# Performance work log

Measured on AMD Instinct MI355X. Metric: run time of the kernel, lower is better.

Reference implementation:

```python
import jax, jax.numpy as jnp
import numpy as np

N = 100000
E = 1200000
F_IN, HID, LAT = 16, 128, 64
G = 8  # number of graphs
SG_K = 4


def setup_inputs() -> dict:
    key = jax.random.key(0)
    ks = jax.random.split(key, 20)
    x = jax.random.normal(ks[0], (N, F_IN), dtype=jnp.float32)
    edge_index = jax.random.randint(ks[1], (2, E), 0, N, dtype=jnp.int64)
    batch = jnp.sort(jax.random.randint(ks[2], (N,), 0, G, dtype=jnp.int64))

    def lin(k, fan_in, fan_out):
        s = 1.0 / np.sqrt(fan_in)
        k1, k2 = jax.random.split(k)
        W = jax.random.uniform(k1, (fan_in, fan_out), jnp.float32, -s, s)
        b = jax.random.uniform(k2, (fan_out,), jnp.float32, -s, s)
        return W, b

    W1, b1 = lin(ks[3], F_IN, HID)
    W2, b2 = lin(ks[4], HID, LAT)
    Wg1, bg1 = lin(ks[5], LAT, LAT)
    Wg2, bg2 = lin(ks[6], LAT, LAT)
    Wg3, bg3 = lin(ks[7], LAT, LAT)
    Wsg, bsg = lin(ks[8], LAT, LAT)
    Wf1, bf1 = lin(ks[9], LAT, 32)
    Wf2, bf2 = lin(ks[10], 32, 16)
    Wc, bc = lin(ks[11], 16, 1)
    Wcb, bcb = lin(ks[12], 16, 1)
    return dict(x=x, edge_index=edge_index, batch=batch,
                W1=W1, b1=b1, W2=W2, b2=b2,
                Wg1=Wg1, bg1=bg1, Wg2=Wg2, bg2=bg2, Wg3=Wg3, bg3=bg3,
                Wsg=Wsg, bsg=bsg, Wf1=Wf1, bf1=bf1, Wf2=Wf2, bf2=bf2,
                Wc=Wc, bc=bc, Wcb=Wcb, bcb=bcb)


def reference(x, edge_index, batch,
              W1, b1, W2, b2,
              Wg1, bg1, Wg2, bg2, Wg3, bg3,
              Wsg, bsg, Wf1, bf1, Wf2, bf2,
              Wc, bc, Wcb, bcb):
    n = x.shape[0]
    loops = jnp.arange(n, dtype=edge_index.dtype)
    src = jnp.concatenate([edge_index[0], loops])  # add self-loops (PyG default)
    dst = jnp.concatenate([edge_index[1], loops])
    deg = jax.ops.segment_sum(jnp.ones_like(dst, jnp.float32), dst, num_segments=n)
    dis = jnp.where(deg > 0, jax.lax.rsqrt(jnp.maximum(deg, 1.0)), 0.0)
    norm = dis[src] * dis[dst]  # symmetric GCN normalization

    def prop(h):
        # D^{-1/2} (A+I) D^{-1/2} h  via gather -> scale -> scatter-add
        return jax.ops.segment_sum(h[src] * norm[:, None], dst, num_segments=n)

    def gcn(h, W, b):
        return prop(h @ W) + b

    # encoder
    z = jax.nn.relu(gcn(x, W1, b1))
    z = gcn(z, W2, b2)
    # stacked GCNs
    z = jax.nn.relu(gcn(z, Wg1, bg1))
    z = jax.nn.relu(gcn(z, Wg2, bg2))
    z = jax.nn.relu(gcn(z, Wg3, bg3))
    # SGConv: propagate K times, then linear
    h = z
    for _ in range(SG_K):
        h = prop(h)
    z = h @ Wsg + bsg
    # global max pool per graph
    g = jax.ops.segment_max(z, batch, num_segments=G)
    g = jax.nn.relu(g @ Wf1 + bf1)
    g = jax.nn.relu(g @ Wf2 + bf2)
    cpd_pred = g @ Wc + bc
    comb_logits = g @ Wcb + bcb
    return cpd_pred, comb_logits
```

## Files before the change

kernel.cpp:

```cpp
#include <hip/hip_runtime.h>
#include <hip/hip_bf16.h>
#include <hip/hip_fp16.h>
#include <math.h>

#define G_GRAPHS 8

__device__ __forceinline__ unsigned fmap(float f) {
    unsigned b = __float_as_uint(f);
    return (b & 0x80000000u) ? ~b : (b | 0x80000000u);
}
__device__ __forceinline__ float funmap(unsigned u) {
    unsigned b = (u & 0x80000000u) ? (u & 0x7fffffffu) : ~u;
    return __uint_as_float(b);
}
__device__ __forceinline__ void fma_row(float wv, uint2 r,
                                        float& ax, float& ay, float& az, float& aw) {
    float2 f01 = __half22float2(*(__half2*)&r.x);
    float2 f23 = __half22float2(*(__half2*)&r.y);
    ax += wv * f01.x; ay += wv * f01.y; az += wv * f23.x; aw += wv * f23.y;
}
__device__ __forceinline__ uint2 pack4(float ax, float ay, float az, float aw) {
    __half2 p01 = __float22half2_rn(make_float2(ax, ay));
    __half2 p23 = __float22half2_rn(make_float2(az, aw));
    uint2 r;
    r.x = *(unsigned*)&p01;
    r.y = *(unsigned*)&p23;
    return r;
}

__global__ void k_count(const int* __restrict__ dst, int* __restrict__ deg, int E) {
    int e = blockIdx.x * 256 + threadIdx.x;
    if (e < E) atomicAdd(&deg[dst[e]], 1);
}

__global__ void k_dis(const int* __restrict__ deg, float* __restrict__ dis, int N) {
    int i = blockIdx.x * 256 + threadIdx.x;
    if (i < N) dis[i] = rsqrtf((float)(deg[i] + 1));
}

__global__ void k_scanA(const int* __restrict__ deg, int* __restrict__ rowst,
                        int* __restrict__ bsum, int N) {
    __shared__ int s[256];
    int i = blockIdx.x * 256 + threadIdx.x;
    int v = (i < N) ? deg[i] : 0;
    s[threadIdx.x] = v;
    __syncthreads();
    for (int off = 1; off < 256; off <<= 1) {
        int t = (threadIdx.x >= off) ? s[threadIdx.x - off] : 0;
        __syncthreads();
        s[threadIdx.x] += t;
        __syncthreads();
    }
    if (i < N) rowst[i] = s[threadIdx.x] - v;
    if (threadIdx.x == 255) bsum[blockIdx.x] = s[255];
}

__global__ void k_scanB(int* __restrict__ bsum, int NB) {
    __shared__ int s[512];
    int t = threadIdx.x;
    int v = (t < NB) ? bsum[t] : 0;
    s[t] = v;
    __syncthreads();
    for (int off = 1; off < 512; off <<= 1) {
        int x = (t >= off) ? s[t - off] : 0;
        __syncthreads();
        s[t] += x;
        __syncthreads();
    }
    if (t < NB) bsum[t] = s[t] - v;
}

__global__ void k_scanC(int* __restrict__ rowst, const int* __restrict__ bsum, int N) {
    int i = blockIdx.x * 256 + threadIdx.x;
    if (i < N) rowst[i] += bsum[blockIdx.x];
}

__global__ void k_fill(const int* __restrict__ src, const int* __restrict__ dst,
                       const float* __restrict__ dis, const int* __restrict__ rowst,
                       int* __restrict__ cnt, int2* __restrict__ edge, int E) {
    int e = blockIdx.x * 256 + threadIdx.x;
    if (e >= E) return;
    int d = dst[e], s = src[e];
    int p = rowst[d] + atomicAdd(&cnt[d], 1);
    edge[p] = make_int2(s, __float_as_int(dis[s] * dis[d]));
}

__global__ void k_x2h(const float* __restrict__ x, __half* __restrict__ xh, int n4) {
    int i = blockIdx.x * 256 + threadIdx.x;
    if (i >= n4) return;
    float4 v = ((const float4*)x)[i];
    ((uint2*)xh)[i] = pack4(v.x, v.y, v.z, v.w);
}

__global__ __launch_bounds__(256) void k_prop16(
        const __half* __restrict__ xh, float* __restrict__ out,
        const float* __restrict__ dis, const int* __restrict__ rowst,
        const int* __restrict__ deg, const int2* __restrict__ edge, int N) {
    int t = threadIdx.x, lane = t & 63, w = t >> 6;
    int grp = lane >> 2, sub = lane & 3;
    int node = blockIdx.x * 64 + w * 16 + grp;
    if (node >= N) return;
    const uint2* xr = (const uint2*)xh;
    float d = dis[node];
    float sc = d * d;
    float ax = 0.f, ay = 0.f, az = 0.f, aw = 0.f;
    fma_row(sc, xr[node * 4 + sub], ax, ay, az, aw);
    int s = rowst[node], dg = deg[node];
    const int2* ep = edge + s;
    int i = 0;
    for (; i + 3 < dg; i += 4) {
        int2 e0 = ep[i], e1 = ep[i + 1], e2 = ep[i + 2], e3 = ep[i + 3];
        uint2 r0 = xr[e0.x * 4 + sub];
        uint2 r1 = xr[e1.x * 4 + sub];
        uint2 r2 = xr[e2.x * 4 + sub];
        uint2 r3 = xr[e3.x * 4 + sub];
        fma_row(__int_as_float(e0.y), r0, ax, ay, az, aw);
        fma_row(__int_as_float(e1.y), r1, ax, ay, az, aw);
        fma_row(__int_as_float(e2.y), r2, ax, ay, az, aw);
        fma_row(__int_as_float(e3.y), r3, ax, ay, az, aw);
    }
    for (; i < dg; ++i) {
        int2 e0 = ep[i];
        fma_row(__int_as_float(e0.y), xr[e0.x * 4 + sub], ax, ay, az, aw);
    }
    ((float4*)out)[node * 4 + sub] = make_float4(ax, ay, az, aw);
}

__global__ __launch_bounds__(256) void k_dense(
        const float* __restrict__ p0, __half* __restrict__ out,
        const float* __restrict__ W1, const float* __restrict__ b1,
        const float* __restrict__ W2, int N) {
    __shared__ float zT[4][128][4];
    int t = threadIdx.x, lane = t & 63, w = t >> 6;
    int base = (blockIdx.x * 4 + w) * 4;
    if (base >= N) return;
    float p = p0[base * 16 + lane];
    float zA[4], zB[4];
    float bA = b1[lane], bB = b1[lane + 64];
    #pragma unroll
    for (int j = 0; j < 4; ++j) { zA[j] = bA; zB[j] = bB; }
    #pragma unroll
    for (int k = 0; k < 16; ++k) {
        float w1a = W1[k * 128 + lane];
        float w1b = W1[k * 128 + lane + 64];
        #pragma unroll
        for (int j = 0; j < 4; ++j) {
            float pk = __shfl(p, j * 16 + k);
            zA[j] += pk * w1a;
            zB[j] += pk * w1b;
        }
    }
    #pragma unroll
    for (int j = 0; j < 4; ++j) {
        zT[w][lane][j]      = fmaxf(zA[j], 0.f);
        zT[w][lane + 64][j] = fmaxf(zB[j], 0.f);
    }
    float acc[4] = {0.f, 0.f, 0.f, 0.f};
    #pragma unroll 4
    for (int k = 0; k < 128; ++k) {
        float wk = W2[k * 64 + lane];
        float4 zk = *(const float4*)&zT[w][k][0];
        acc[0] += zk.x * wk; acc[1] += zk.y * wk;
        acc[2] += zk.z * wk; acc[3] += zk.w * wk;
    }
    #pragma unroll
    for (int j = 0; j < 4; ++j)
        if (base + j < N) out[(base + j) * 64 + lane] = __float2half(acc[j]);
}

__global__ __launch_bounds__(256) void k_prop64(
        const __half* __restrict__ in, __half* __restrict__ out,
        const float* __restrict__ dis, const int* __restrict__ rowst,
        const int* __restrict__ deg, const int2* __restrict__ edge,
        const float* __restrict__ bias, int relu,
        const float* __restrict__ W, const float* __restrict__ gbias, int N) {
    __shared__ float Wlds[64 * 64];
    __shared__ float zbuf[4][2][64];
    int t = threadIdx.x, lane = t & 63, w = t >> 6;
    int q = lane & 15, g = lane >> 4;
    const uint2* inr = (const uint2*)in;
    if (W) {
        for (int i = t; i < 64 * 64 / 4; i += 256)
            ((float4*)Wlds)[i] = ((const float4*)W)[i];
        __syncthreads();
    }
    float4 b4 = make_float4(0.f, 0.f, 0.f, 0.f);
    if (bias) b4 = ((const float4*)bias)[q];
    float gb = (W && gbias) ? gbias[lane] : 0.f;
    int wid = blockIdx.x * 4 + w;
    const int stride = gridDim.x * 4 * 2;
    for (int n0 = wid * 2; n0 < N; n0 += stride) {
        int n1 = n0 + 1;
        bool h1 = n1 < N;
        int s0 = rowst[n0], d0 = deg[n0];
        int s1 = h1 ? rowst[n1] : s0, d1 = h1 ? deg[n1] : 0;
        float di0 = dis[n0];
        float di1 = h1 ? dis[n1] : 0.f;
        const int2* e0 = edge + s0;
        const int2* e1 = edge + s1;
        float sc0 = di0 * di0 * 0.25f, sc1 = di1 * di1 * 0.25f;
        float a0x = 0.f, a0y = 0.f, a0z = 0.f, a0w = 0.f;
        float a1x = 0.f, a1y = 0.f, a1z = 0.f, a1w = 0.f;
        fma_row(sc0, inr[n0 * 16 + q], a0x, a0y, a0z, a0w);
        fma_row(sc1, inr[(h1 ? n1 : n0) * 16 + q], a1x, a1y, a1z, a1w);
        int m = d0 > d1 ? d0 : d1;
        for (int base = 0; base < m; base += 16) {
            int i0 = base + g, i1 = i0 + 4, i2 = i0 + 8, i3 = i0 + 12;
            int2 ma0 = e0[(i0 < d0) ? i0 : 0];
            int2 ma1 = e0[(i1 < d0) ? i1 : 0];
            int2 ma2 = e0[(i2 < d0) ? i2 : 0];
            int2 ma3 = e0[(i3 < d0) ? i3 : 0];
            int2 mb0 = e1[(i0 < d1) ? i0 : 0];
            int2 mb1 = e1[(i1 < d1) ? i1 : 0];
            int2 mb2 = e1[(i2 < d1) ? i2 : 0];
            int2 mb3 = e1[(i3 < d1) ? i3 : 0];
            uint2 ra0 = inr[ma0.x * 16 + q];
            uint2 ra1 = inr[ma1.x * 16 + q];
            uint2 ra2 = inr[ma2.x * 16 + q];
            uint2 ra3 = inr[ma3.x * 16 + q];
            uint2 rb0 = inr[mb0.x * 16 + q];
            uint2 rb1 = inr[mb1.x * 16 + q];
            uint2 rb2 = inr[mb2.x * 16 + q];
            uint2 rb3 = inr[mb3.x * 16 + q];
            float wa0 = (i0 < d0) ? __int_as_float(ma0.y) : 0.f;
            float wa1 = (i1 < d0) ? __int_as_float(ma1.y) : 0.f;
            float wa2 = (i2 < d0) ? __int_as_float(ma2.y) : 0.f;
            float wa3 = (i3 < d0) ? __int_as_float(ma3.y) : 0.f;
            float wb0 = (i0 < d1) ? __int_as_float(mb0.y) : 0.f;
            float wb1 = (i1 < d1) ? __int_as_float(mb1.y) : 0.f;
            float wb2 = (i2 < d1) ? __int_as_float(mb2.y) : 0.f;
            float wb3 = (i3 < d1) ? __int_as_float(mb3.y) : 0.f;
            fma_row(wa0, ra0, a0x, a0y, a0z, a0w);
            fma_row(wa1, ra1, a0x, a0y, a0z, a0w);
            fma_row(wa2, ra2, a0x, a0y, a0z, a0w);
            fma_row(wa3, ra3, a0x, a0y, a0z, a0w);
            fma_row(wb0, rb0, a1x, a1y, a1z, a1w);
            fma_row(wb1, rb1, a1x, a1y, a1z, a1w);
            fma_row(wb2, rb2, a1x, a1y, a1z, a1w);
            fma_row(wb3, rb3, a1x, a1y, a1z, a1w);
        }
        a0x += __shfl_xor(a0x,16); a0y += __shfl_xor(a0y,16); a0z += __shfl_xor(a0z,16); a0w += __shfl_xor(a0w,16);
        a0x += __shfl_xor(a0x,32); a0y += __shfl_xor(a0y,32); a0z += __shfl_xor(a0z,32); a0w += __shfl_xor(a0w,32);
        a1x += __shfl_xor(a1x,16); a1y += __shfl_xor(a1y,16); a1z += __shfl_xor(a1z,16); a1w += __shfl_xor(a1w,16);
        a1x += __shfl_xor(a1x,32); a1y += __shfl_xor(a1y,32); a1z += __shfl_xor(a1z,32); a1w += __shfl_xor(a1w,32);
        a0x += b4.x; a0y += b4.y; a0z += b4.z; a0w += b4.w;
        a1x += b4.x; a1y += b4.y; a1z += b4.z; a1w += b4.w;
        if (relu) {
            a0x = fmaxf(a0x,0.f); a0y = fmaxf(a0y,0.f); a0z = fmaxf(a0z,0.f); a0w = fmaxf(a0w,0.f);
            a1x = fmaxf(a1x,0.f); a1y = fmaxf(a1y,0.f); a1z = fmaxf(a1z,0.f); a1w = fmaxf(a1w,0.f);
        }
        if (!W) {
            if (g == 0) {
                ((uint2*)out)[n0 * 16 + q] = pack4(a0x, a0y, a0z, a0w);
                if (h1) ((uint2*)out)[n1 * 16 + q] = pack4(a1x, a1y, a1z, a1w);
            }
        } else {
            if (g == 0) {
                ((float4*)zbuf[w][0])[q] = make_float4(a0x, a0y, a0z, a0w);
                ((float4*)zbuf[w][1])[q] = make_float4(a1x, a1y, a1z, a1w);
            }
            float acc0 = gb, acc1 = gb;
            for (int k = 0; k < 64; ++k) {
                float wk = Wlds[k * 64 + lane];
                acc0 += zbuf[w][0][k] * wk;
                acc1 += zbuf[w][1][k] * wk;
            }
            out[n0 * 64 + lane] = __float2half(acc0);
            if (h1) out[n1 * 64 + lane] = __float2half(acc1);
        }
    }
}

__global__ void k_pool_init(unsigned* __restrict__ gmax) {
    gmax[blockIdx.x * 64 + threadIdx.x] = fmap(-INFINITY);
}

__global__ void k_pool(const __half* __restrict__ z, const int* __restrict__ batch,
                       unsigned* __restrict__ gmax, int N) {
    int f = threadIdx.x & 63, w = threadIdx.x >> 6;
    int base = (blockIdx.x * 4 + w) * 32;
    if (base >= N) return;
    int end = base + 32; if (end > N) end = N;
    int b0 = batch[base], b1 = batch[end - 1];
    if (b0 == b1) {
        float lmax = -INFINITY;
        for (int n = base; n < end; ++n)
            lmax = fmaxf(lmax, __half2float(z[n * 64 + f]));
        atomicMax(&gmax[b0 * 64 + f], fmap(lmax));
    } else {
        int curb = b0; float lmax = -INFINITY;
        for (int n = base; n < end; ++n) {
            int b = batch[n];
            if (b != curb) {
                atomicMax(&gmax[curb * 64 + f], fmap(lmax));
                curb = b; lmax = -INFINITY;
            }
            lmax = fmaxf(lmax, __half2float(z[n * 64 + f]));
        }
        atomicMax(&gmax[curb * 64 + f], fmap(lmax));
    }
}

__global__ void k_head(const unsigned* __restrict__ gmax,
                       const float* __restrict__ Wf1, const float* __restrict__ bf1,
                       const float* __restrict__ Wf2, const float* __restrict__ bf2,
                       const float* __restrict__ Wc, const float* __restrict__ bc,
                       const float* __restrict__ Wcb, const float* __restrict__ bcb,
                       float* __restrict__ out) {
    __shared__ float g[8][64], h1[8][32], h2[8][16];
    int t = threadIdx.x;
    for (int i = t; i < 512; i += 64) g[i >> 6][i & 63] = funmap(gmax[i]);
    __syncthreads();
    for (int i = t; i < 256; i += 64) {
        int r = i >> 5, c = i & 31;
        float a = bf1[c];
        for (int k = 0; k < 64; ++k) a += g[r][k] * Wf1[k * 32 + c];
        h1[r][c] = fmaxf(a, 0.f);
    }
    __syncthreads();
    for (int i = t; i < 128; i += 64) {
        int r = i >> 4, c = i & 15;
        float a = bf2[c];
        for (int k = 0; k < 32; ++k) a += h1[r][k] * Wf2[k * 16 + c];
        h2[r][c] = fmaxf(a, 0.f);
    }
    __syncthreads();
    if (t < 16) {
        int r = t & 7;
        bool comb = t >= 8;
        const float* W = comb ? Wcb : Wc;
// ... 12 lines not shown
    const float* W1   = (const float*)d_in[3];
    const float* b1   = (const float*)d_in[4];
    const float* W2   = (const float*)d_in[5];
    const float* b2   = (const float*)d_in[6];
    const float* Wg1  = (const float*)d_in[7];
    const float* bg1  = (const float*)d_in[8];
    const float* Wg2  = (const float*)d_in[9];
    const float* bg2  = (const float*)d_in[10];
    const float* Wg3  = (const float*)d_in[11];
    const float* bg3  = (const float*)d_in[12];
    const float* Wsg  = (const float*)d_in[13];
    const float* bsg  = (const float*)d_in[14];
    const float* Wf1  = (const float*)d_in[15];
    const float* bf1  = (const float*)d_in[16];
    const float* Wf2  = (const float*)d_in[17];
    const float* bf2  = (const float*)d_in[18];
    const float* Wc   = (const float*)d_in[19];
    const float* bc   = (const float*)d_in[20];
    const float* Wcb  = (const float*)d_in[21];
    const float* bcb  = (const float*)d_in[22];

    const int N = in_sizes[0] / 16;
    const int E = in_sizes[1] / 2;
    const int* esrc = ei;
    const int* edst = ei + E;

    char* ws = (char*)d_ws;
    auto alloc = [&](size_t bytes) -> char* {
        char* p = ws;
        ws += (bytes + 255) & ~(size_t)255;
        return p;
    };
    int*      deg   = (int*)alloc((size_t)N * 4);
    int*      cnt   = (int*)alloc((size_t)N * 4);
    int*      rowst = (int*)alloc((size_t)(N + 1) * 4);
    int*      bsum  = (int*)alloc(4096);
    float*    dis   = (float*)alloc((size_t)N * 4);
    int2*     edge  = (int2*)alloc((size_t)(E + 16) * 8);
    __half*   xh    = (__half*)alloc((size_t)N * 16 * 2);
    float*    p0    = (float*)alloc((size_t)N * 16 * 4);
    __half*   bufA  = (__half*)alloc((size_t)N * 64 * 2);
    __half*   bufB  = (__half*)alloc((size_t)N * 64 * 2);
    unsigned* gmax  = (unsigned*)alloc((size_t)G_GRAPHS * 64 * 4);

    hipMemsetAsync(deg, 0, (size_t)N * 4, stream);
    hipMemsetAsync(cnt, 0, (size_t)N * 4, stream);
    hipMemsetAsync(edge + E, 0, 16 * 8, stream);

    const int EB = (E + 255) / 256;
    const int NB = (N + 255) / 256;
    const int PB = 2048;

    k_count<<<EB, 256, 0, stream>>>(edst, deg, E);
    k_dis<<<NB, 256, 0, stream>>>(deg, dis, N);
    k_scanA<<<NB, 256, 0, stream>>>(deg, rowst, bsum, N);
    k_scanB<<<1, 512, 0, stream>>>(bsum, NB);
    k_scanC<<<NB, 256, 0, stream>>>(rowst, bsum, N);
    k_fill<<<EB, 256, 0, stream>>>(esrc, edst, dis, rowst, cnt, edge, E);
    k_x2h<<<(N * 4 + 255) / 256, 256, 0, stream>>>(x, xh, N * 4);

    k_prop16<<<(N + 63) / 64, 256, 0, stream>>>(xh, p0, dis, rowst, deg, edge, N);
    k_dense<<<(N + 15) / 16, 256, 0, stream>>>(p0, bufA, W1, b1, W2, N);
    k_prop64<<<PB, 256, 0, stream>>>(bufA, bufB, dis, rowst, deg, edge, b2, 0, Wg1, nullptr, N);
    k_prop64<<<PB, 256, 0, stream>>>(bufB, bufA, dis, rowst, deg, edge, bg1, 1, Wg2, nullptr, N);
    k_prop64<<<PB, 256, 0, stream>>>(bufA, bufB, dis, rowst, deg, edge, bg2, 1, Wg3, nullptr, N);
    k_prop64<<<PB, 256, 0, stream>>>(bufB, bufA, dis, rowst, deg, edge, bg3, 1, nullptr, nullptr, N);
    k_prop64<<<PB, 256, 0, stream>>>(bufA, bufB, dis, rowst, deg, edge, nullptr, 0, nullptr, nullptr, N);
    k_prop64<<<PB, 256, 0, stream>>>(bufB, bufA, dis, rowst, deg, edge, nullptr, 0, nullptr, nullptr, N);
    k_prop64<<<PB, 256, 0, stream>>>(bufA, bufB, dis, rowst, deg, edge, nullptr, 0, nullptr, nullptr, N);
    k_prop64<<<PB, 256, 0, stream>>>(bufB, bufA, dis, rowst, deg, edge, nullptr, 0, Wsg, bsg, N);

    k_pool_init<<<G_GRAPHS, 64, 0, stream>>>(gmax);
    k_pool<<<(N + 127) / 128, 256, 0, stream>>>(bufA, batch, gmax, N);
    k_head<<<1, 64, 0, stream>>>(gmax, Wf1, bf1, Wf2, bf2, Wc, bc, Wcb, bcb, (float*)d_out);
}
```

Measured before the change: 610.5 us.

## Slice features into 16-wide planes, fold self-loops into CSR, split GEMM from propagation

Feature buffers change from row-major 64-wide rows to four 16-feature planes. Propagation runs per slice (block index selects the slice), so each gather touches a smaller, more cache-friendly array. Self-loops become explicit CSR entries, so one generic propagation kernel handles every layer, and the 16-wide first-layer output is now stored in half precision. The fused propagate+matmul kernel is split into a separate propagation kernel and a standalone 64x64 GEMM kernel. This adds extra kernel launches and intermediate traffic, and re-reads the edge list four times per layer.

```diff
diff --git a/kernel.cpp b/kernel.cpp
--- a/kernel.cpp
+++ b/kernel.cpp
@@ -1,5 +1,4 @@
 #include <hip/hip_runtime.h>
-#include <hip/hip_bf16.h>
 #include <hip/hip_fp16.h>
 #include <math.h>
 
@@ -33,16 +32,21 @@
     if (e < E) atomicAdd(&deg[dst[e]], 1);
 }
 
-__global__ void k_dis(const int* __restrict__ deg, float* __restrict__ dis, int N) {
-    int i = blockIdx.x * 256 + threadIdx.x;
-    if (i < N) dis[i] = rsqrtf((float)(deg[i] + 1));
+__global__ void k_dis(const int* __restrict__ deg, float* __restrict__ dis,
+                      int* __restrict__ degp, int N) {
+    int i = blockIdx.x * 256 + threadIdx.x;
+    if (i < N) {
+        int d = deg[i];
+        dis[i] = rsqrtf((float)(d + 1));
+        degp[i] = d + 1;
+    }
 }
 
 __global__ void k_scanA(const int* __restrict__ deg, int* __restrict__ rowst,
                         int* __restrict__ bsum, int N) {
     __shared__ int s[256];
     int i = blockIdx.x * 256 + threadIdx.x;
-    int v = (i < N) ? deg[i] : 0;
+    int v = (i < N) ? deg[i] + 1 : 0;
     s[threadIdx.x] = v;
     __syncthreads();
     for (int off = 1; off < 256; off <<= 1) {
@@ -73,6 +77,15 @@
 __global__ void k_scanC(int* __restrict__ rowst, const int* __restrict__ bsum, int N) {
     int i = blockIdx.x * 256 + threadIdx.x;
     if (i < N) rowst[i] += bsum[blockIdx.x];
+}
+
+__global__ void k_self(const int* __restrict__ rowst, const int* __restrict__ deg,
+                       int2* __restrict__ edge, int N) {
+    int i = blockIdx.x * 256 + threadIdx.x;
+    if (i < N) {
+        float sw = 1.0f / (float)(deg[i] + 1);
+        edge[rowst[i]] = make_int2(i, __float_as_int(sw));
+    }
 }
 
 __global__ void k_fill(const int* __restrict__ src, const int* __restrict__ dst,
@@ -81,7 +94,7 @@
     int e = blockIdx.x * 256 + threadIdx.x;
     if (e >= E) return;
     int d = dst[e], s = src[e];
-    int p = rowst[d] + atomicAdd(&cnt[d], 1);
+    int p = rowst[d] + 1 + atomicAdd(&cnt[d], 1);
     edge[p] = make_int2(s, __float_as_int(dis[s] * dis[d]));
 }
 
@@ -92,49 +105,67 @@
     ((uint2*)xh)[i] = pack4(v.x, v.y, v.z, v.w);
 }
 
-__global__ __launch_bounds__(256) void k_prop16(
-        const __half* __restrict__ xh, float* __restrict__ out,
-        const float* __restrict__ dis, const int* __restrict__ rowst,
-        const int* __restrict__ deg, const int2* __restrict__ edge, int N) {
+__global__ __launch_bounds__(256) void k_prop(
+        const __half* __restrict__ in, __half* __restrict__ out,
+        const int* __restrict__ rowst, const int* __restrict__ degp,
+        const int2* __restrict__ edge,
+        const float* __restrict__ bias, int relu, int N,
+        int smask, int sshift) {
     int t = threadIdx.x, lane = t & 63, w = t >> 6;
-    int grp = lane >> 2, sub = lane & 3;
-    int node = blockIdx.x * 64 + w * 16 + grp;
-    if (node >= N) return;
-    const uint2* xr = (const uint2*)xh;
-    float d = dis[node];
-    float sc = d * d;
-    float ax = 0.f, ay = 0.f, az = 0.f, aw = 0.f;
-    fma_row(sc, xr[node * 4 + sub], ax, ay, az, aw);
-    int s = rowst[node], dg = deg[node];
-    const int2* ep = edge + s;
-    int i = 0;
-    for (; i + 3 < dg; i += 4) {
-        int2 e0 = ep[i], e1 = ep[i + 1], e2 = ep[i + 2], e3 = ep[i + 3];
-        uint2 r0 = xr[e0.x * 4 + sub];
-        uint2 r1 = xr[e1.x * 4 + sub];
-        uint2 r2 = xr[e2.x * 4 + sub];
-        uint2 r3 = xr[e3.x * 4 + sub];
-        fma_row(__int_as_float(e0.y), r0, ax, ay, az, aw);
-        fma_row(__int_as_float(e1.y), r1, ax, ay, az, aw);
-        fma_row(__int_as_float(e2.y), r2, ax, ay, az, aw);
-        fma_row(__int_as_float(e3.y), r3, ax, ay, az, aw);
-    }
-    for (; i < dg; ++i) {
-        int2 e0 = ep[i];
-        fma_row(__int_as_float(e0.y), xr[e0.x * 4 + sub], ax, ay, az, aw);
-    }
-    ((float4*)out)[node * 4 + sub] = make_float4(ax, ay, az, aw);
+    int sub = lane & 3, eg = (lane >> 2) & 7, n2 = lane >> 5;
+    int slice = blockIdx.x & smask;
+    int sbid = blockIdx.x >> sshift;
+    int nslots = (gridDim.x >> sshift) * 4;
+    size_t NP16 = (size_t)N * 16;
+    const __half* inp = in + (size_t)slice * NP16;
+    __half* outp = out + (size_t)slice * NP16;
+    float4 b4 = make_float4(0.f, 0.f, 0.f, 0.f);
+    if (bias) b4 = *(const float4*)&bias[slice * 16 + sub * 4];
+    int pairs = (N + 1) >> 1;
+    for (int p = sbid * 4 + w; p < pairs; p += nslots) {
+        int node = p * 2 + n2;
+        bool ok = node < N;
+        int s = ok ? rowst[node] : 0;
+        int d = ok ? degp[node] : 0;
+        const int2* ep = edge + s;
+        float a0 = 0.f, a1 = 0.f, a2 = 0.f, a3 = 0.f;
+        for (int base = 0; base < d; base += 16) {
+            int i0 = base + eg, i1 = base + eg + 8;
+            long long m0 = __builtin_nontemporal_load(
+                (const long long*)(ep + ((i0 < d) ? i0 : 0)));
+            long long m1 = __builtin_nontemporal_load(
+                (const long long*)(ep + ((i1 < d) ? i1 : 0)));
+            int c0 = (int)(m0 & 0xffffffffLL);
+            int c1 = (int)(m1 & 0xffffffffLL);
+            float w0 = (i0 < d) ? __int_as_float((int)(m0 >> 32)) : 0.f;
+            float w1 = (i1 < d) ? __int_as_float((int)(m1 >> 32)) : 0.f;
+            uint2 r0 = *(const uint2*)&inp[(size_t)c0 * 16 + sub * 4];
+            uint2 r1 = *(const uint2*)&inp[(size_t)c1 * 16 + sub * 4];
+            fma_row(w0, r0, a0, a1, a2, a3);
+            fma_row(w1, r1, a0, a1, a2, a3);
+        }
+        a0 += __shfl_xor(a0, 4);  a1 += __shfl_xor(a1, 4);  a2 += __shfl_xor(a2, 4);  a3 += __shfl_xor(a3, 4);
+        a0 += __shfl_xor(a0, 8);  a1 += __shfl_xor(a1, 8);  a2 += __shfl_xor(a2, 8);  a3 += __shfl_xor(a3, 8);
+        a0 += __shfl_xor(a0, 16); a1 += __shfl_xor(a1, 16); a2 += __shfl_xor(a2, 16); a3 += __shfl_xor(a3, 16);
+        a0 += b4.x; a1 += b4.y; a2 += b4.z; a3 += b4.w;
+        if (relu) {
+            a0 = fmaxf(a0, 0.f); a1 = fmaxf(a1, 0.f);
+            a2 = fmaxf(a2, 0.f); a3 = fmaxf(a3, 0.f);
+        }
+        if (eg == 0 && ok)
+            *(uint2*)&outp[(size_t)node * 16 + sub * 4] = pack4(a0, a1, a2, a3);
+    }
 }
 
 __global__ __launch_bounds__(256) void k_dense(
-        const float* __restrict__ p0, __half* __restrict__ out,
+        const __half* __restrict__ p0h, __half* __restrict__ out,
         const float* __restrict__ W1, const float* __restrict__ b1,
         const float* __restrict__ W2, int N) {
     __shared__ float zT[4][128][4];
     int t = threadIdx.x, lane = t & 63, w = t >> 6;
     int base = (blockIdx.x * 4 + w) * 4;
     if (base >= N) return;
-    float p = p0[base * 16 + lane];
+    float p = __half2float(p0h[(size_t)base * 16 + lane]);
     float zA[4], zB[4];
     float bA = b1[lane], bB = b1[lane + 64];
     #pragma unroll
@@ -163,111 +194,52 @@
         acc[0] += zk.x * wk; acc[1] += zk.y * wk;
         acc[2] += zk.z * wk; acc[3] += zk.w * wk;
     }
+    size_t NP16 = (size_t)N * 16;
+    size_t po = (size_t)(lane >> 4) * NP16 + (lane & 15);
     #pragma unroll
     for (int j = 0; j < 4; ++j)
-        if (base + j < N) out[(base + j) * 64 + lane] = __float2half(acc[j]);
-}
-
-__global__ __launch_bounds__(256) void k_prop64(
+        if (base + j < N)
+            out[po + (size_t)(base + j) * 16] = __float2half(acc[j]);
+}
+
+__global__ __launch_bounds__(256) void k_gemm64(
         const __half* __restrict__ in, __half* __restrict__ out,
-        const float* __restrict__ dis, const int* __restrict__ rowst,
-        const int* __restrict__ deg, const int2* __restrict__ edge,
-        const float* __restrict__ bias, int relu,
         const float* __restrict__ W, const float* __restrict__ gbias, int N) {
     __shared__ float Wlds[64 * 64];
-    __shared__ float zbuf[4][2][64];
+    __shared__ float zs[8][64];
     int t = threadIdx.x, lane = t & 63, w = t >> 6;
-    int q = lane & 15, g = lane >> 4;
-    const uint2* inr = (const uint2*)in;
-    if (W) {
-        for (int i = t; i < 64 * 64 / 4; i += 256)
-            ((float4*)Wlds)[i] = ((const float4*)W)[i];
-        __syncthreads();
-    }
-    float4 b4 = make_float4(0.f, 0.f, 0.f, 0.f);
-    if (bias) b4 = ((const float4*)bias)[q];
-    float gb = (W && gbias) ? gbias[lane] : 0.f;
-    int wid = blockIdx.x * 4 + w;
-    const int stride = gridDim.x * 4 * 2;
-    for (int n0 = wid * 2; n0 < N; n0 += stride) {
-        int n1 = n0 + 1;
-        bool h1 = n1 < N;
-        int s0 = rowst[n0], d0 = deg[n0];
-        int s1 = h1 ? rowst[n1] : s0, d1 = h1 ? deg[n1] : 0;
-        float di0 = dis[n0];
-        float di1 = h1 ? dis[n1] : 0.f;
-        const int2* e0 = edge + s0;
-        const int2* e1 = edge + s1;
-        float sc0 = di0 * di0 * 0.25f, sc1 = di1 * di1 * 0.25f;
-        float a0x = 0.f, a0y = 0.f, a0z = 0.f, a0w = 0.f;
-        float a1x = 0.f, a1y = 0.f, a1z = 0.f, a1w = 0.f;
-        fma_row(sc0, inr[n0 * 16 + q], a0x, a0y, a0z, a0w);
-        fma_row(sc1, inr[(h1 ? n1 : n0) * 16 + q], a1x, a1y, a1z, a1w);
-        int m = d0 > d1 ? d0 : d1;
-        for (int base = 0; base < m; base += 16) {
-            int i0 = base + g, i1 = i0 + 4, i2 = i0 + 8, i3 = i0 + 12;
-            int2 ma0 = e0[(i0 < d0) ? i0 : 0];
-            int2 ma1 = e0[(i1 < d0) ? i1 : 0];
-            int2 ma2 = e0[(i2 < d0) ? i2 : 0];
-            int2 ma3 = e0[(i3 < d0) ? i3 : 0];
-            int2 mb0 = e1[(i0 < d1) ? i0 : 0];
-            int2 mb1 = e1[(i1 < d1) ? i1 : 0];
-            int2 mb2 = e1[(i2 < d1) ? i2 : 0];
-            int2 mb3 = e1[(i3 < d1) ? i3 : 0];
-            uint2 ra0 = inr[ma0.x * 16 + q];
-            uint2 ra1 = inr[ma1.x * 16 + q];
-            uint2 ra2 = inr[ma2.x * 16 + q];
-            uint2 ra3 = inr[ma3.x * 16 + q];
-            uint2 rb0 = inr[mb0.x * 16 + q];
-            uint2 rb1 = inr[mb1.x * 16 + q];
-            uint2 rb2 = inr[mb2.x * 16 + q];
-            uint2 rb3 = inr[mb3.x * 16 + q];
-            float wa0 = (i0 < d0) ? __int_as_float(ma0.y) : 0.f;
-            float wa1 = (i1 < d0) ? __int_as_float(ma1.y) : 0.f;
-            float wa2 = (i2 < d0) ? __int_as_float(ma2.y) : 0.f;
-            float wa3 = (i3 < d0) ? __int_as_float(ma3.y) : 0.f;
-            float wb0 = (i0 < d1) ? __int_as_float(mb0.y) : 0.f;
-            float wb1 = (i1 < d1) ? __int_as_float(mb1.y) : 0.f;
-            float wb2 = (i2 < d1) ? __int_as_float(mb2.y) : 0.f;
-            float wb3 = (i3 < d1) ? __int_as_float(mb3.y) : 0.f;
-            fma_row(wa0, ra0, a0x, a0y, a0z, a0w);
-            fma_row(wa1, ra1, a0x, a0y, a0z, a0w);
-            fma_row(wa2, ra2, a0x, a0y, a0z, a0w);
-            fma_row(wa3, ra3, a0x, a0y, a0z, a0w);
-            fma_row(wb0, rb0, a1x, a1y, a1z, a1w);
-            fma_row(wb1, rb1, a1x, a1y, a1z, a1w);
-            fma_row(wb2, rb2, a1x, a1y, a1z, a1w);
-            fma_row(wb3, rb3, a1x, a1y, a1z, a1w);
-        }
-        a0x += __shfl_xor(a0x,16); a0y += __shfl_xor(a0y,16); a0z += __shfl_xor(a0z,16); a0w += __shfl_xor(a0w,16);
-        a0x += __shfl_xor(a0x,32); a0y += __shfl_xor(a0y,32); a0z += __shfl_xor(a0z,32); a0w += __shfl_xor(a0w,32);
-        a1x += __shfl_xor(a1x,16); a1y += __shfl_xor(a1y,16); a1z += __shfl_xor(a1z,16); a1w += __shfl_xor(a1w,16);
-        a1x += __shfl_xor(a1x,32); a1y += __shfl_xor(a1y,32); a1z += __shfl_xor(a1z,32); a1w += __shfl_xor(a1w,32);
-        a0x += b4.x; a0y += b4.y; a0z += b4.z; a0w += b4.w;
-        a1x += b4.x; a1y += b4.y; a1z += b4.z; a1w += b4.w;
-        if (relu) {
-            a0x = fmaxf(a0x,0.f); a0y = fmaxf(a0y,0.f); a0z = fmaxf(a0z,0.f); a0w = fmaxf(a0w,0.f);
-            a1x = fmaxf(a1x,0.f); a1y = fmaxf(a1y,0.f); a1z = fmaxf(a1z,0.f); a1w = fmaxf(a1w,0.f);
-        }
-        if (!W) {
-            if (g == 0) {
-                ((uint2*)out)[n0 * 16 + q] = pack4(a0x, a0y, a0z, a0w);
-                if (h1) ((uint2*)out)[n1 * 16 + q] = pack4(a1x, a1y, a1z, a1w);
-            }
-        } else {
-            if (g == 0) {
-                ((float4*)zbuf[w][0])[q] = make_float4(a0x, a0y, a0z, a0w);
-                ((float4*)zbuf[w][1])[q] = make_float4(a1x, a1y, a1z, a1w);
-            }
-            float acc0 = gb, acc1 = gb;
-            for (int k = 0; k < 64; ++k) {
-                float wk = Wlds[k * 64 + lane];
-                acc0 += zbuf[w][0][k] * wk;
-                acc1 += zbuf[w][1][k] * wk;
-            }
-            out[n0 * 64 + lane] = __float2half(acc0);
-            if (h1) out[n1 * 64 + lane] = __float2half(acc1);
-        }
+    for (int i = t; i < 64 * 64 / 4; i += 256)
+        ((float4*)Wlds)[i] = ((const float4*)W)[i];
+    __syncthreads();
+    float gb = gbias ? gbias[lane] : 0.f;
+    size_t NP16 = (size_t)N * 16;
+    int groups = (N + 7) >> 3;
+    int nl = t >> 5, u = t & 31;
+    int ss = u >> 3, dp = u & 7;
+    for (int gi = blockIdx.x; gi < groups; gi += gridDim.x) {
+        int base = gi * 8;
+        {
+            int node = base + nl;
+            unsigned v = 0;
+            if (node < N)
+                v = *(const unsigned*)&in[(size_t)ss * NP16 + (size_t)node * 16 + dp * 2];
+            float2 f = __half22float2(*(__half2*)&v);
+            zs[nl][ss * 16 + dp * 2]     = f.x;
+            zs[nl][ss * 16 + dp * 2 + 1] = f.y;
+        }
+        __syncthreads();
+        int n0 = base + w * 2, n1 = n0 + 1;
+        float acc0 = gb, acc1 = gb;
+        #pragma unroll 8
+        for (int k = 0; k < 64; ++k) {
+            float wk = Wlds[k * 64 + lane];
+            acc0 += zs[w * 2][k] * wk;
+            acc1 += zs[w * 2 + 1][k] * wk;
+        }
+        size_t po = (size_t)(lane >> 4) * NP16 + (lane & 15);
+        if (n0 < N) out[po + (size_t)n0 * 16] = __float2half(acc0);
+        if (n1 < N) out[po + (size_t)n1 * 16] = __float2half(acc1);
+        __syncthreads();
     }
 }
 
@@ -281,11 +253,13 @@
     int base = (blockIdx.x * 4 + w) * 32;
     if (base >= N) return;
     int end = base + 32; if (end > N) end = N;
+    size_t NP16 = (size_t)N * 16;
+    const __half* zf = z + (size_t)(f >> 4) * NP16 + (f & 15);
     int b0 = batch[base], b1 = batch[end - 1];
     if (b0 == b1) {
         float lmax = -INFINITY;
         for (int n = base; n < end; ++n)
-            lmax = fmaxf(lmax, __half2float(z[n * 64 + f]));
+            lmax = fmaxf(lmax, __half2float(zf[(size_t)n * 16]));
         atomicMax(&gmax[b0 * 64 + f], fmap(lmax));
     } else {
         int curb = b0; float lmax = -INFINITY;
@@ -295,7 +269,7 @@
                 atomicMax(&gmax[curb * 64 + f], fmap(lmax));
                 curb = b; lmax = -INFINITY;
             }
-            lmax = fmaxf(lmax, __half2float(z[n * 64 + f]));
+            lmax = fmaxf(lmax, __half2float(zf[(size_t)n * 16]));
         }
         atomicMax(&gmax[curb * 64 + f], fmap(lmax));
     }
@@ -374,43 +348,49 @@
         return p;
     };
     int*      deg   = (int*)alloc((size_t)N * 4);
+    int*      degp  = (int*)alloc((size_t)N * 4);
     int*      cnt   = (int*)alloc((size_t)N * 4);
     int*      rowst = (int*)alloc((size_t)(N + 1) * 4);
     int*      bsum  = (int*)alloc(4096);
     float*    dis   = (float*)alloc((size_t)N * 4);
-    int2*     edge  = (int2*)alloc((size_t)(E + 16) * 8);
+    int2*     edge  = (int2*)alloc((size_t)(E + N + 16) * 8);
     __half*   xh    = (__half*)alloc((size_t)N * 16 * 2);
-    float*    p0    = (float*)alloc((size_t)N * 16 * 4);
+    __half*   p0h   = (__half*)alloc((size_t)N * 16 * 2);
     __half*   bufA  = (__half*)alloc((size_t)N * 64 * 2);
     __half*   bufB  = (__half*)alloc((size_t)N * 64 * 2);
     unsigned* gmax  = (unsigned*)alloc((size_t)G_GRAPHS * 64 * 4);
 
     hipMemsetAsync(deg, 0, (size_t)N * 4, stream);
     hipMemsetAsync(cnt, 0, (size_t)N * 4, stream);
-    hipMemsetAsync(edge + E, 0, 16 * 8, stream);
 
     const int EB = (E + 255) / 256;
     const int NB = (N + 255) / 256;
     const int PB = 2048;
+    const int GB = 1024;
 
     k_count<<<EB, 256, 0, stream>>>(edst, deg, E);
-    k_dis<<<NB, 256, 0, stream>>>(deg, dis, N);
+    k_dis<<<NB, 256, 0, stream>>>(deg, dis, degp, N);
     k_scanA<<<NB, 256, 0, stream>>>(deg, rowst, bsum, N);
     k_scanB<<<1, 512, 0, stream>>>(bsum, NB);
     k_scanC<<<NB, 256, 0, stream>>>(rowst, bsum, N);
+    k_self<<<NB, 256, 0, stream>>>(rowst, deg, edge, N);
     k_fill<<<EB, 256, 0, stream>>>(esrc, edst, dis, rowst, cnt, edge, E);
     k_x2h<<<(N * 4 + 255) / 256, 256, 0, stream>>>(x, xh, N * 4);
 
-    k_prop16<<<(N + 63) / 64, 256, 0, stream>>>(xh, p0, dis, rowst, deg, edge, N);
-    k_dense<<<(N + 15) / 16, 256, 0, stream>>>(p0, bufA, W1, b1, W2, N);
-    k_prop64<<<PB, 256, 0, stream>>>(bufA, bufB, dis, rowst, deg, edge, b2, 0, Wg1, nullptr, N);
-    k_prop64<<<PB, 256, 0, stream>>>(bufB, bufA, dis, rowst, deg, edge, bg1, 1, Wg2, nullptr, N);
-    k_prop64<<<PB, 256, 0, stream>>>(bufA, bufB, dis, rowst, deg, edge, bg2, 1, Wg3, nullptr, N);
-    k_prop64<<<PB, 256, 0, stream>>>(bufB, bufA, dis, rowst, deg, edge, bg3, 1, nullptr, nullptr, N);
-    k_prop64<<<PB, 256, 0, stream>>>(bufA, bufB, dis, rowst, deg, edge, nullptr, 0, nullptr, nullptr, N);
-    k_prop64<<<PB, 256, 0, stream>>>(bufB, bufA, dis, rowst, deg, edge, nullptr, 0, nullptr, nullptr, N);
-    k_prop64<<<PB, 256, 0, stream>>>(bufA, bufB, dis, rowst, deg, edge, nullptr, 0, nullptr, nullptr, N);
-    k_prop64<<<PB, 256, 0, stream>>>(bufB, bufA, dis, rowst, deg, edge, nullptr, 0, Wsg, bsg, N);
+    k_prop<<<PB, 256, 0, stream>>>(xh, p0h, rowst, degp, edge, nullptr, 0, N, 0, 0);
+    k_dense<<<(N + 15) / 16, 256, 0, stream>>>(p0h, bufA, W1, b1, W2, N);
+    k_prop<<<PB, 256, 0, stream>>>(bufA, bufB, rowst, degp, edge, b2, 0, N, 3, 2);
+    k_gemm64<<<GB, 256, 0, stream>>>(bufB, bufA, Wg1, nullptr, N);
+    k_prop<<<PB, 256, 0, stream>>>(bufA, bufB, rowst, degp, edge, bg1, 1, N, 3, 2);
+    k_gemm64<<<GB, 256, 0, stream>>>(bufB, bufA, Wg2, nullptr, N);
+    k_prop<<<PB, 256, 0, stream>>>(bufA, bufB, rowst, degp, edge, bg2, 1, N, 3, 2);
+    k_gemm64<<<GB, 256, 0, stream>>>(bufB, bufA, Wg3, nullptr, N);
+    k_prop<<<PB, 256, 0, stream>>>(bufA, bufB, rowst, degp, edge, bg3, 1, N, 3, 2);
+    k_prop<<<PB, 256, 0, stream>>>(bufB, bufA, rowst, degp, edge, nullptr, 0, N, 3, 2);
+    k_prop<<<PB, 256, 0, stream>>>(bufA, bufB, rowst, degp, edge, nullptr, 0, N, 3, 2);
+    k_prop<<<PB, 256, 0, stream>>>(bufB, bufA, rowst, degp, edge, nullptr, 0, N, 3, 2);
+    k_prop<<<PB, 256, 0, stream>>>(bufA, bufB, rowst, degp, edge, nullptr, 0, N, 3, 2);
+    k_gemm64<<<GB, 256, 0, stream>>>(bufB, bufA, Wsg, bsg, N);
 
     k_pool_init<<<G_GRAPHS, 64, 0, stream>>>(gmax);
     k_pool<<<(N + 127) / 128, 256, 0, stream>>>(bufA, batch, gmax, N);
```

Measured after the change: 944.0 us. 1.55x slower.

## Fold self-loops into CSR, use nontemporal edge loads and fp16 weights in LDS

Applied to the files above, without the earlier changes.

Self-loop edges are now stored at the start of each CSR row with weight 1/(deg+1), so the propagation kernels no longer do a separate self-term gather or read dis. Edge records are fetched with nontemporal loads, presumably to avoid polluting cache needed for feature gathers. The fused dense weights are packed as half2 in dynamic shared memory, halving LDS footprint, and the kernel is templated on whether a weight matrix is present. The CSR grows by N entries and the weights lose precision in the fused matmul.

```diff
diff --git a/kernel.cpp b/kernel.cpp
--- a/kernel.cpp
+++ b/kernel.cpp
@@ -1,5 +1,4 @@
 #include <hip/hip_runtime.h>
-#include <hip/hip_bf16.h>
 #include <hip/hip_fp16.h>
 #include <math.h>
 
@@ -33,16 +32,21 @@
     if (e < E) atomicAdd(&deg[dst[e]], 1);
 }
 
-__global__ void k_dis(const int* __restrict__ deg, float* __restrict__ dis, int N) {
+__global__ void k_dis(const int* __restrict__ deg, float* __restrict__ dis,
+                      int* __restrict__ degp, int N) {
     int i = blockIdx.x * 256 + threadIdx.x;
-    if (i < N) dis[i] = rsqrtf((float)(deg[i] + 1));
+    if (i < N) {
+        int d = deg[i];
+        dis[i] = rsqrtf((float)(d + 1));
+        degp[i] = d + 1;
+    }
 }
 
 __global__ void k_scanA(const int* __restrict__ deg, int* __restrict__ rowst,
                         int* __restrict__ bsum, int N) {
     __shared__ int s[256];
     int i = blockIdx.x * 256 + threadIdx.x;
-    int v = (i < N) ? deg[i] : 0;
+    int v = (i < N) ? deg[i] + 1 : 0;
     s[threadIdx.x] = v;
     __syncthreads();
     for (int off = 1; off < 256; off <<= 1) {
@@ -75,13 +79,22 @@
     if (i < N) rowst[i] += bsum[blockIdx.x];
 }
 
+__global__ void k_self(const int* __restrict__ rowst, const int* __restrict__ deg,
+                       int2* __restrict__ edge, int N) {
+    int i = blockIdx.x * 256 + threadIdx.x;
+    if (i < N) {
+        float sw = 1.0f / (float)(deg[i] + 1);
+        edge[rowst[i]] = make_int2(i, __float_as_int(sw));
+    }
+}
+
 __global__ void k_fill(const int* __restrict__ src, const int* __restrict__ dst,
                        const float* __restrict__ dis, const int* __restrict__ rowst,
                        int* __restrict__ cnt, int2* __restrict__ edge, int E) {
     int e = blockIdx.x * 256 + threadIdx.x;
     if (e >= E) return;
     int d = dst[e], s = src[e];
-    int p = rowst[d] + atomicAdd(&cnt[d], 1);
+    int p = rowst[d] + 1 + atomicAdd(&cnt[d], 1);
     edge[p] = make_int2(s, __float_as_int(dis[s] * dis[d]));
 }
 
@@ -94,34 +107,34 @@
 
 __global__ __launch_bounds__(256) void k_prop16(
         const __half* __restrict__ xh, float* __restrict__ out,
-        const float* __restrict__ dis, const int* __restrict__ rowst,
-        const int* __restrict__ deg, const int2* __restrict__ edge, int N) {
+        const int* __restrict__ rowst, const int* __restrict__ degp,
+        const int2* __restrict__ edge, int N) {
     int t = threadIdx.x, lane = t & 63, w = t >> 6;
     int grp = lane >> 2, sub = lane & 3;
     int node = blockIdx.x * 64 + w * 16 + grp;
     if (node >= N) return;
     const uint2* xr = (const uint2*)xh;
-    float d = dis[node];
-    float sc = d * d;
     float ax = 0.f, ay = 0.f, az = 0.f, aw = 0.f;
-    fma_row(sc, xr[node * 4 + sub], ax, ay, az, aw);
-    int s = rowst[node], dg = deg[node];
+    int s = rowst[node], d = degp[node];
     const int2* ep = edge + s;
-    int i = 0;
-    for (; i + 3 < dg; i += 4) {
-        int2 e0 = ep[i], e1 = ep[i + 1], e2 = ep[i + 2], e3 = ep[i + 3];
-        uint2 r0 = xr[e0.x * 4 + sub];
-        uint2 r1 = xr[e1.x * 4 + sub];
-        uint2 r2 = xr[e2.x * 4 + sub];
-        uint2 r3 = xr[e3.x * 4 + sub];
-        fma_row(__int_as_float(e0.y), r0, ax, ay, az, aw);
-        fma_row(__int_as_float(e1.y), r1, ax, ay, az, aw);
-        fma_row(__int_as_float(e2.y), r2, ax, ay, az, aw);
-        fma_row(__int_as_float(e3.y), r3, ax, ay, az, aw);
-    }
-    for (; i < dg; ++i) {
-        int2 e0 = ep[i];
-        fma_row(__int_as_float(e0.y), xr[e0.x * 4 + sub], ax, ay, az, aw);
+    for (int i = 0; i < d; i += 4) {
+        int j0 = i, j1 = i + 1, j2 = i + 2, j3 = i + 3;
+        long long m0 = __builtin_nontemporal_load((const long long*)(ep + j0));
+        long long m1 = __builtin_nontemporal_load((const long long*)(ep + ((j1 < d) ? j1 : 0)));
+        long long m2 = __builtin_nontemporal_load((const long long*)(ep + ((j2 < d) ? j2 : 0)));
+        long long m3 = __builtin_nontemporal_load((const long long*)(ep + ((j3 < d) ? j3 : 0)));
+        uint2 r0 = xr[(size_t)(int)(m0 & 0xffffffffLL) * 4 + sub];
+        uint2 r1 = xr[(size_t)(int)(m1 & 0xffffffffLL) * 4 + sub];
+        uint2 r2 = xr[(size_t)(int)(m2 & 0xffffffffLL) * 4 + sub];
+        uint2 r3 = xr[(size_t)(int)(m3 & 0xffffffffLL) * 4 + sub];
+        float w0 = __int_as_float((int)(m0 >> 32));
+        float w1 = (j1 < d) ? __int_as_float((int)(m1 >> 32)) : 0.f;
+        float w2 = (j2 < d) ? __int_as_float((int)(m2 >> 32)) : 0.f;
+        float w3 = (j3 < d) ? __int_as_float((int)(m3 >> 32)) : 0.f;
+        fma_row(w0, r0, ax, ay, az, aw);
+        fma_row(w1, r1, ax, ay, az, aw);
+        fma_row(w2, r2, ax, ay, az, aw);
+        fma_row(w3, r3, ax, ay, az, aw);
     }
     ((float4*)out)[node * 4 + sub] = make_float4(ax, ay, az, aw);
 }
@@ -134,7 +147,7 @@
     int t = threadIdx.x, lane = t & 63, w = t >> 6;
     int base = (blockIdx.x * 4 + w) * 4;
     if (base >= N) return;
-    float p = p0[base * 16 + lane];
+    float p = p0[(size_t)base * 16 + lane];
     float zA[4], zB[4];
     float bA = b1[lane], bB = b1[lane + 64];
     #pragma unroll
@@ -165,71 +178,76 @@
     }
     #pragma unroll
     for (int j = 0; j < 4; ++j)
-        if (base + j < N) out[(base + j) * 64 + lane] = __float2half(acc[j]);
-}
-
+        if (base + j < N) out[(size_t)(base + j) * 64 + lane] = __float2half(acc[j]);
+}
+
+template<bool HASW>
 __global__ __launch_bounds__(256) void k_prop64(
         const __half* __restrict__ in, __half* __restrict__ out,
-        const float* __restrict__ dis, const int* __restrict__ rowst,
-        const int* __restrict__ deg, const int2* __restrict__ edge,
+        const int* __restrict__ rowst, const int* __restrict__ degp,
+        const int2* __restrict__ edge,
         const float* __restrict__ bias, int relu,
         const float* __restrict__ W, const float* __restrict__ gbias, int N) {
-    __shared__ float Wlds[64 * 64];
-    __shared__ float zbuf[4][2][64];
+    extern __shared__ char smem[];
+    unsigned* Whl = (unsigned*)smem;
+    float* zb = (float*)(smem + 8192);
     int t = threadIdx.x, lane = t & 63, w = t >> 6;
     int q = lane & 15, g = lane >> 4;
     const uint2* inr = (const uint2*)in;
-    if (W) {
-        for (int i = t; i < 64 * 64 / 4; i += 256)
-            ((float4*)Wlds)[i] = ((const float4*)W)[i];
+    if (HASW) {
+        for (int i = t; i < 2048; i += 256) {
+            int kk = i >> 6, l = i & 63;
+            __half2 h = __floats2half2_rn(make_float2(W[(2 * kk) * 64 + l],
+                                                      W[(2 * kk + 1) * 64 + l]).x,
+                                          make_float2(W[(2 * kk) * 64 + l],
+                                                      W[(2 * kk + 1) * 64 + l]).y);
+            __half2 hh; hh.x = __float2half(W[(2 * kk) * 64 + l]);
+            hh.y = __float2half(W[(2 * kk + 1) * 64 + l]);
+            Whl[i] = *(unsigned*)&hh;
+        }
         __syncthreads();
     }
     float4 b4 = make_float4(0.f, 0.f, 0.f, 0.f);
     if (bias) b4 = ((const float4*)bias)[q];
-    float gb = (W && gbias) ? gbias[lane] : 0.f;
+    float gb = (HASW && gbias) ? gbias[lane] : 0.f;
     int wid = blockIdx.x * 4 + w;
     const int stride = gridDim.x * 4 * 2;
     for (int n0 = wid * 2; n0 < N; n0 += stride) {
         int n1 = n0 + 1;
         bool h1 = n1 < N;
-        int s0 = rowst[n0], d0 = deg[n0];
-        int s1 = h1 ? rowst[n1] : s0, d1 = h1 ? deg[n1] : 0;
-        float di0 = dis[n0];
-        float di1 = h1 ? dis[n1] : 0.f;
+        int s0 = rowst[n0], d0 = degp[n0];
+        int s1 = h1 ? rowst[n1] : s0, d1 = h1 ? degp[n1] : 0;
         const int2* e0 = edge + s0;
         const int2* e1 = edge + s1;
-        float sc0 = di0 * di0 * 0.25f, sc1 = di1 * di1 * 0.25f;
         float a0x = 0.f, a0y = 0.f, a0z = 0.f, a0w = 0.f;
         float a1x = 0.f, a1y = 0.f, a1z = 0.f, a1w = 0.f;
-        fma_row(sc0, inr[n0 * 16 + q], a0x, a0y, a0z, a0w);
-        fma_row(sc1, inr[(h1 ? n1 : n0) * 16 + q], a1x, a1y, a1z, a1w);
         int m = d0 > d1 ? d0 : d1;
         for (int base = 0; base < m; base += 16) {
             int i0 = base + g, i1 = i0 + 4, i2 = i0 + 8, i3 = i0 + 12;
-            int2 ma0 = e0[(i0 < d0) ? i0 : 0];
-            int2 ma1 = e0[(i1 < d0) ? i1 : 0];
-            int2 ma2 = e0[(i2 < d0) ? i2 : 0];
-            int2 ma3 = e0[(i3 < d0) ? i3 : 0];
-            int2 mb0 = e1[(i0 < d1) ? i0 : 0];
-            int2 mb1 = e1[(i1 < d1) ? i1 : 0];
-            int2 mb2 = e1[(i2 < d1) ? i2 : 0];
-            int2 mb3 = e1[(i3 < d1) ? i3 : 0];
-            uint2 ra0 = inr[ma0.x * 16 + q];
-            uint2 ra1 = inr[ma1.x * 16 + q];
-            uint2 ra2 = inr[ma2.x * 16 + q];
-            uint2 ra3 = inr[ma3.x * 16 + q];
-            uint2 rb0 = inr[mb0.x * 16 + q];
-            uint2 rb1 = inr[mb1.x * 16 + q];
-            uint2 rb2 = inr[mb2.x * 16 + q];
-            uint2 rb3 = inr[mb3.x * 16 + q];
-            float wa0 = (i0 < d0) ? __int_as_float(ma0.y) : 0.f;
-            float wa1 = (i1 < d0) ? __int_as_float(ma1.y) : 0.f;
-            float wa2 = (i2 < d0) ? __int_as_float(ma2.y) : 0.f;
-            float wa3 = (i3 < d0) ? __int_as_float(ma3.y) : 0.f;
-            float wb0 = (i0 < d1) ? __int_as_float(mb0.y) : 0.f;
-            float wb1 = (i1 < d1) ? __int_as_float(mb1.y) : 0.f;
-            float wb2 = (i2 < d1) ? __int_as_float(mb2.y) : 0.f;
-            float wb3 = (i3 < d1) ? __int_as_float(mb3.y) : 0.f;
+            long long ma0 = __builtin_nontemporal_load((const long long*)(e0 + ((i0 < d0) ? i0 : 0)));
+            long long ma1 = __builtin_nontemporal_load((const long long*)(e0 + ((i1 < d0) ? i1 : 0)));
+            long long ma2 = __builtin_nontemporal_load((const long long*)(e0 + ((i2 < d0) ? i2 : 0)));
+            long long ma3 = __builtin_nontemporal_load((const long long*)(e0 + ((i3 < d0) ? i3 : 0)));
+            long long mb0 = __builtin_nontemporal_load((const long long*)(e1 + ((i0 < d1) ? i0 : 0)));
+            long long mb1 = __builtin_nontemporal_load((const long long*)(e1 + ((i1 < d1) ? i1 : 0)));
+            long long mb2 = __builtin_nontemporal_load((const long long*)(e1 + ((i2 < d1) ? i2 : 0)));
+            long long mb3 = __builtin_nontemporal_load((const long long*)(e1 + ((i3 < d1) ? i3 : 0)));
+            uint2 ra0 = inr[(size_t)(int)(ma0 & 0xffffffffLL) * 16 + q];
+            uint2 ra1 = inr[(size_t)(int)(ma1 & 0xffffffffLL) * 16 + q];
+            uint2 ra2 = inr[(size_t)(int)(ma2 & 0xffffffffLL) * 16 + q];
+            uint2 ra3 = inr[(size_t)(int)(ma3 & 0xffffffffLL) * 16 + q];
+            uint2 rb0 = inr[(size_t)(int)(mb0 & 0xffffffffLL) * 16 + q];
+            uint2 rb1 = inr[(size_t)(int)(mb1 & 0xffffffffLL) * 16 + q];
+            uint2 rb2 = inr[(size_t)(int)(mb2 & 0xffffffffLL) * 16 + q];
+            uint2 rb3 = inr[(size_t)(int)(mb3 & 0xffffffffLL) * 16 + q];
+            float wa0 = (i0 < d0) ? __int_as_float((int)(ma0 >> 32)) : 0.f;
+            float wa1 = (i1 < d0) ? __int_as_float((int)(ma1 >> 32)) : 0.f;
+            float wa2 = (i2 < d0) ? __int_as_float((int)(ma2 >> 32)) : 0.f;
+            float wa3 = (i3 < d0) ? __int_as_float((int)(ma3 >> 32)) : 0.f;
+            float wb0 = (i0 < d1) ? __int_as_float((int)(mb0 >> 32)) : 0.f;
+            float wb1 = (i1 < d1) ? __int_as_float((int)(mb1 >> 32)) : 0.f;
+            float wb2 = (i2 < d1) ? __int_as_float((int)(mb2 >> 32)) : 0.f;
+            float wb3 = (i3 < d1) ? __int_as_float((int)(mb3 >> 32)) : 0.f;
             fma_row(wa0, ra0, a0x, a0y, a0z, a0w);
             fma_row(wa1, ra1, a0x, a0y, a0z, a0w);
             fma_row(wa2, ra2, a0x, a0y, a0z, a0w);
@@ -249,24 +267,28 @@
             a0x = fmaxf(a0x,0.f); a0y = fmaxf(a0y,0.f); a0z = fmaxf(a0z,0.f); a0w = fmaxf(a0w,0.f);
             a1x = fmaxf(a1x,0.f); a1y = fmaxf(a1y,0.f); a1z = fmaxf(a1z,0.f); a1w = fmaxf(a1w,0.f);
         }
-        if (!W) {
+        if (!HASW) {
             if (g == 0) {
-                ((uint2*)out)[n0 * 16 + q] = pack4(a0x, a0y, a0z, a0w);
-                if (h1) ((uint2*)out)[n1 * 16 + q] = pack4(a1x, a1y, a1z, a1w);
+                ((uint2*)out)[(size_t)n0 * 16 + q] = pack4(a0x, a0y, a0z, a0w);
+                if (h1) ((uint2*)out)[(size_t)n1 * 16 + q] = pack4(a1x, a1y, a1z, a1w);
             }
         } else {
             if (g == 0) {
-                ((float4*)zbuf[w][0])[q] = make_float4(a0x, a0y, a0z, a0w);
-                ((float4*)zbuf[w][1])[q] = make_float4(a1x, a1y, a1z, a1w);
+                ((float4*)&zb[(w * 2 + 0) * 64])[q] = make_float4(a0x, a0y, a0z, a0w);
+                ((float4*)&zb[(w * 2 + 1) * 64])[q] = make_float4(a1x, a1y, a1z, a1w);
             }
             float acc0 = gb, acc1 = gb;
-            for (int k = 0; k < 64; ++k) {
-                float wk = Wlds[k * 64 + lane];
-                acc0 += zbuf[w][0][k] * wk;
-                acc1 += zbuf[w][1][k] * wk;
+            #pragma unroll 8
+            for (int kk = 0; kk < 32; ++kk) {
+                unsigned u = Whl[kk * 64 + lane];
+                float2 wp = __half22float2(*(__half2*)&u);
+                float2 z0 = *(float2*)&zb[(w * 2 + 0) * 64 + 2 * kk];
+                float2 z1 = *(float2*)&zb[(w * 2 + 1) * 64 + 2 * kk];
+                acc0 += z0.x * wp.x + z0.y * wp.y;
+                acc1 += z1.x * wp.x + z1.y * wp.y;
             }
-            out[n0 * 64 + lane] = __float2half(acc0);
-            if (h1) out[n1 * 64 + lane] = __float2half(acc1);
+            out[(size_t)n0 * 64 + lane] = __float2half(acc0);
+            if (h1) out[(size_t)n1 * 64 + lane] = __float2half(acc1);
         }
     }
 }
@@ -285,7 +307,7 @@
     if (b0 == b1) {
         float lmax = -INFINITY;
         for (int n = base; n < end; ++n)
-            lmax = fmaxf(lmax, __half2float(z[n * 64 + f]));
+            lmax = fmaxf(lmax, __half2float(z[(size_t)n * 64 + f]));
         atomicMax(&gmax[b0 * 64 + f], fmap(lmax));
     } else {
         int curb = b0; float lmax = -INFINITY;
@@ -295,7 +317,7 @@
                 atomicMax(&gmax[curb * 64 + f], fmap(lmax));
                 curb = b; lmax = -INFINITY;
             }
-            lmax = fmaxf(lmax, __half2float(z[n * 64 + f]));
+            lmax = fmaxf(lmax, __half2float(z[(size_t)n * 64 + f]));
         }
         atomicMax(&gmax[curb * 64 + f], fmap(lmax));
     }
@@ -374,11 +396,12 @@
         return p;
     };
     int*      deg   = (int*)alloc((size_t)N * 4);
+    int*      degp  = (int*)alloc((size_t)N * 4);
     int*      cnt   = (int*)alloc((size_t)N * 4);
     int*      rowst = (int*)alloc((size_t)(N + 1) * 4);
     int*      bsum  = (int*)alloc(4096);
     float*    dis   = (float*)alloc((size_t)N * 4);
-    int2*     edge  = (int2*)alloc((size_t)(E + 16) * 8);
+    int2*     edge  = (int2*)alloc((size_t)(E + N + 16) * 8);
     __half*   xh    = (__half*)alloc((size_t)N * 16 * 2);
     float*    p0    = (float*)alloc((size_t)N * 16 * 4);
     __half*   bufA  = (__half*)alloc((size_t)N * 64 * 2);
@@ -387,30 +410,31 @@
 
     hipMemsetAsync(deg, 0, (size_t)N * 4, stream);
     hipMemsetAsync(cnt, 0, (size_t)N * 4, stream);
-    hipMemsetAsync(edge + E, 0, 16 * 8, stream);
 
     const int EB = (E + 255) / 256;
     const int NB = (N + 255) / 256;
     const int PB = 2048;
+    const size_t SW = 10240;
 
     k_count<<<EB, 256, 0, stream>>>(edst, deg, E);
-    k_dis<<<NB, 256, 0, stream>>>(deg, dis, N);
+    k_dis<<<NB, 256, 0, stream>>>(deg, dis, degp, N);
     k_scanA<<<NB, 256, 0, stream>>>(deg, rowst, bsum, N);
     k_scanB<<<1, 512, 0, stream>>>(bsum, NB);
     k_scanC<<<NB, 256, 0, stream>>>(rowst, bsum, N);
+    k_self<<<NB, 256, 0, stream>>>(rowst, deg, edge, N);
     k_fill<<<EB, 256, 0, stream>>>(esrc, edst, dis, rowst, cnt, edge, E);
     k_x2h<<<(N * 4 + 255) / 256, 256, 0, stream>>>(x, xh, N * 4);
 
-    k_prop16<<<(N + 63) / 64, 256, 0, stream>>>(xh, p0, dis, rowst, deg, edge, N);
+    k_prop16<<<(N + 63) / 64, 256, 0, stream>>>(xh, p0, rowst, degp, edge, N);
     k_dense<<<(N + 15) / 16, 256, 0, stream>>>(p0, bufA, W1, b1, W2, N);
-    k_prop64<<<PB, 256, 0, stream>>>(bufA, bufB, dis, rowst, deg, edge, b2, 0, Wg1, nullptr, N);
-    k_prop64<<<PB, 256, 0, stream>>>(bufB, bufA, dis, rowst, deg, edge, bg1, 1, Wg2, nullptr, N);
-    k_prop64<<<PB, 256, 0, stream>>>(bufA, bufB, dis, rowst, deg, edge, bg2, 1, Wg3, nullptr, N);
-    k_prop64<<<PB, 256, 0, stream>>>(bufB, bufA, dis, rowst, deg, edge, bg3, 1, nullptr, nullptr, N);
-    k_prop64<<<PB, 256, 0, stream>>>(bufA, bufB, dis, rowst, deg, edge, nullptr, 0, nullptr, nullptr, N);
-    k_prop64<<<PB, 256, 0, stream>>>(bufB, bufA, dis, rowst, deg, edge, nullptr, 0, nullptr, nullptr, N);
-    k_prop64<<<PB, 256, 0, stream>>>(bufA, bufB, dis, rowst, deg, edge, nullptr, 0, nullptr, nullptr, N);
-    k_prop64<<<PB, 256, 0, stream>>>(bufB, bufA, dis, rowst, deg, edge, nullptr, 0, Wsg, bsg, N);
+    k_prop64<true><<<PB, 256, SW, stream>>>(bufA, bufB, rowst, degp, edge, b2, 0, Wg1, nullptr, N);
+    k_prop64<true><<<PB, 256, SW, stream>>>(bufB, bufA, rowst, degp, edge, bg1, 1, Wg2, nullptr, N);
+    k_prop64<true><<<PB, 256, SW, stream>>>(bufA, bufB, rowst, degp, edge, bg2, 1, Wg3, nullptr, N);
+    k_prop64<false><<<PB, 256, 0, stream>>>(bufB, bufA, rowst, degp, edge, bg3, 1, nullptr, nullptr, N);
+    k_prop64<false><<<PB, 256, 0, stream>>>(bufA, bufB, rowst, degp, edge, nullptr, 0, nullptr, nullptr, N);
+    k_prop64<false><<<PB, 256, 0, stream>>>(bufB, bufA, rowst, degp, edge, nullptr, 0, nullptr, nullptr, N);
+    k_prop64<false><<<PB, 256, 0, stream>>>(bufA, bufB, rowst, degp, edge, nullptr, 0, nullptr, nullptr, N);
+    k_prop64<true><<<PB, 256, SW, stream>>>(bufB, bufA, rowst, degp, edge, nullptr, 0, Wsg, bsg, N);
 
     k_pool_init<<<G_GRAPHS, 64, 0, stream>>>(gmax);
     k_pool<<<(N + 127) / 128, 256, 0, stream>>>(bufA, batch, gmax, N);
```

New measurement: 672.1 us. 1.1x slower.
